# Kernel optimization log

Measured on AMD Instinct MI355X. Metric: run time of the kernel, lower is better.

## Reference

```python
import jax, jax.numpy as jnp
import numpy as np

H = 512          # hidden_size
FP = 256         # feature_padding
E = 512          # embedding_dim
NF = 768         # number of feature embeddings; num_features = NF + FP
L, B = 512, 32   # max_len, batch


def setup_inputs() -> dict:
    key = jax.random.key(0)
    ks = jax.random.split(key, 7)
    s = 0.02
    return {
        "feature_embeddings": jax.random.normal(ks[0], (NF, E), jnp.float32),
        "encoder_outputs": jax.random.normal(ks[1], (L, B, 2 * H), jnp.float32),
        "W_lin": jax.random.normal(ks[2], (H, 2 * H), jnp.float32) * s,   # linear_attn.weight
        "b_lin": jax.random.normal(ks[3], (H,), jnp.float32) * s,         # linear_attn.bias
        "W_feat": jax.random.normal(ks[4], (E, 2 * H), jnp.float32) * s,  # feature_attn.weight
        "b_feat": jax.random.normal(ks[5], (E,), jnp.float32) * s,        # feature_attn.bias
        "v": jax.random.normal(ks[6], (FP, H), jnp.float32) * s,          # self.v
    }


def reference(feature_embeddings, encoder_outputs, W_lin, b_lin, W_feat, b_feat, v):
    # encoder_outputs: [L, B, 2H]
    wh = jnp.einsum('lbi,hi->lbh', encoder_outputs, W_lin) + b_lin      # [L,B,H]
    vwh = jnp.einsum('fh,lbh->lbf', v, wh)                              # [L,B,FP]
    wh2 = jnp.einsum('lbi,ei->lbe', encoder_outputs, W_feat) + b_feat   # [L,B,E]
    fwh = jnp.einsum('ne,lbe->lbn', feature_embeddings, wh2)            # [L,B,NF]
    energy = jnp.concatenate([fwh, vwh], axis=-1)                       # [L,B,NF+FP]
    attn = jax.nn.softmax(energy, axis=-1)                              # softmax over features
    # attn_energies was [B, L, N]; .transpose(1,2) -> [B, N, L]
    return jnp.transpose(attn, (1, 2, 0))
```

## Files before the change

kernel.cpp:

```cpp
#include <hip/hip_runtime.h>
#include <hip/hip_bf16.h>
#include <math.h>

#define Hd   512
#define FPd  256
#define Ed   512
#define NFd  768
#define Ld   512
#define Bd   32
#define K2H  1024
#define Nd   1024
#define Md   (Ld * Bd)

typedef _Float16 f16x8  __attribute__((ext_vector_type(8)));
typedef _Float16 f16x4  __attribute__((ext_vector_type(4)));
typedef float    f32x4  __attribute__((ext_vector_type(4)));
typedef float    f32x16 __attribute__((ext_vector_type(16)));

__global__ __launch_bounds__(256)
void build_wpack(const float* __restrict__ F,
                 const float* __restrict__ Wf,
                 const float* __restrict__ V,
                 const float* __restrict__ Wl,
                 _Float16* __restrict__ Bh) {
    __shared__ float fs[32][64];
    __shared__ float wtile[32][36];
    const int tid = threadIdx.x;
    const int kx  = blockIdx.x;
    const int ny  = blockIdx.y;
    const int n0  = ny * 32;
    const int kl  = tid & 31;
    const int k   = kx * 32 + kl;
    const int ty  = tid >> 5;

    const float* src;  const float* wsrc;
    if (n0 < NFd) { src = F + (size_t)n0 * Ed;          wsrc = Wf; }
    else          { src = V + (size_t)(n0 - NFd) * Hd;  wsrc = Wl; }

    float acc[4];
#pragma unroll
    for (int i = 0; i < 4; i++) acc[i] = 0.f;

    for (int e0 = 0; e0 < 512; e0 += 64) {
#pragma unroll
        for (int rep = 0; rep < 2; rep++) {
            int idx = rep * 256 + tid;
            int i   = idx >> 4;
            int kq  = idx & 15;
            float4 v4 = *(const float4*)(src + (size_t)i * 512 + e0 + kq * 4);
            *(float4*)(&fs[i][kq * 4]) = v4;
        }
        __syncthreads();
#pragma unroll 4
        for (int kk = 0; kk < 64; kk += 4) {
            float w0 = wsrc[(size_t)(e0 + kk + 0) * K2H + k];
            float w1 = wsrc[(size_t)(e0 + kk + 1) * K2H + k];
            float w2 = wsrc[(size_t)(e0 + kk + 2) * K2H + k];
            float w3 = wsrc[(size_t)(e0 + kk + 3) * K2H + k];
#pragma unroll
            for (int i = 0; i < 4; i++) {
                float4 f4 = *(const float4*)(&fs[ty * 4 + i][kk]);
                acc[i] += f4.x * w0 + f4.y * w1 + f4.z * w2 + f4.w * w3;
            }
        }
        __syncthreads();
    }
#pragma unroll
    for (int i = 0; i < 4; i++) wtile[ty * 4 + i][kl] = acc[i];
    __syncthreads();
    if (tid < 128) {
        const int lane = tid & 63;
        const int ksl  = tid >> 6;
        const int nl   = lane & 31;
        const int kf   = ksl * 16 + (lane >> 5) * 8;
        float w[8];
        *(float4*)(w)     = *(const float4*)(&wtile[nl][kf]);
        *(float4*)(w + 4) = *(const float4*)(&wtile[nl][kf + 4]);
        f16x8 h;
#pragma unroll
        for (int j = 0; j < 8; j++) h[j] = (_Float16)w[j];
        const size_t fo = ((size_t)((ny * 64) + (kx * 2 + ksl)) * 64 + lane) * 8;
        *(f16x8*)(Bh + fo) = h;
    }
}

__global__ __launch_bounds__(64)
void build_bias(const float* __restrict__ F, const float* __restrict__ bf,
                const float* __restrict__ V, const float* __restrict__ bl,
                float* __restrict__ bias) {
    const int n    = blockIdx.x;
    const int lane = threadIdx.x;
    const float* row; const float* bsrc;
    if (n < NFd) { row = F + (size_t)n * Ed;          bsrc = bf; }
    else         { row = V + (size_t)(n - NFd) * Hd;  bsrc = bl; }
    float a = 0.f;
#pragma unroll
    for (int rep = 0; rep < 8; rep++) {
        int e = rep * 64 + lane;
        a += row[e] * bsrc[e];
    }
#pragma unroll
    for (int off = 1; off < 64; off <<= 1) a += __shfl_xor(a, off);
    if (lane == 0) bias[n] = a;
}

__global__ __launch_bounds__(1024)
void gemm_direct(const float* __restrict__ enc,
                 const _Float16* __restrict__ Bh,
                 const float* __restrict__ bias,
                 float* __restrict__ out) {
    __shared__ char AsB[2][8192];
    __shared__ float red[16][64];
    __shared__ float redc[64];

    const int tid  = threadIdx.x;
    const int lane = tid & 63;
    const int wn   = tid >> 6;
    const int hf   = lane >> 5;
    const int l31  = lane & 31;
    const int b    = blockIdx.x >> 3;
    const int l0   = (blockIdx.x & 7) * 64;

    float bv[2];
#pragma unroll
    for (int nt = 0; nt < 2; nt++) bv[nt] = bias[wn * 64 + nt * 32 + l31];
    f32x16 acc[2][2];
#pragma unroll
    for (int ms = 0; ms < 2; ms++)
#pragma unroll
        for (int nt = 0; nt < 2; nt++)
#pragma unroll
            for (int r = 0; r < 16; r++) acc[ms][nt][r] = bv[nt];

    const int srow = tid >> 4;
    const int skf  = (tid & 15) * 4;
    const float* gA = enc + ((size_t)(l0 + srow) * Bd + b) * K2H + skf;

    const int kk_w   = skf >> 4;
    const int lh_w   = (skf & 15) >> 3;
    const int j0_w   = skf & 7;
    const int lane_w = lh_w * 32 + (srow & 31);
    const int slot_w = lane_w ^ ((lane_w >> 3) & 7) ^ kk_w;
    const uint32_t wb = (uint32_t)((srow >> 5) * 4096 + kk_w * 1024 + slot_w * 16 + j0_w * 2);

    const uint32_t rb16 = (uint32_t)((lane ^ ((lane >> 3) & 7)) << 4);

    const _Float16* Bp0 = Bh + ((size_t)(wn * 2 + 0) * 64 * 64 + lane) * 8;
    const _Float16* Bp1 = Bh + ((size_t)(wn * 2 + 1) * 64 * 64 + lane) * 8;

#define STAGE_CHUNK(dst, p)                                               \
    {                                                                     \
        f16x4 h_;                                                         \
        _Pragma("unroll")                                                 \
        for (int j = 0; j < 4; j++) h_[j] = (_Float16)((p)[j]);           \
        *(f16x4*)((dst) + wb) = h_;                                       \
    }

    {
        f32x4 p0 = *(const f32x4*)gA;
        STAGE_CHUNK(AsB[0], p0)
    }
    f32x4 pf1 = *(const f32x4*)(gA + 64);
    f16x8 b_cur0 = *(const f16x8*)(Bp0);
    f16x8 b_cur1 = *(const f16x8*)(Bp1);

    for (int c = 0; c < 16; ++c) {
        __syncthreads();
        f32x4 pf2;
        if (c < 14) pf2 = *(const f32x4*)(gA + (c + 2) * 64);
        const char* hbase = AsB[c & 1];
#pragma unroll
        for (int kk = 0; kk < 4; ++kk) {
            const uint32_t ko = (uint32_t)(kk * 1024) + (rb16 ^ (uint32_t)(kk << 4));
            f16x8 a_h[2];
#pragma unroll
            for (int ms = 0; ms < 2; ms++)
                a_h[ms] = *(const f16x8*)(hbase + ms * 4096 + ko);
            int t = c * 4 + kk + 1;
            if (t > 63) t = 63;
            f16x8 b_nxt0 = *(const f16x8*)(Bp0 + (size_t)t * 512);
            f16x8 b_nxt1 = *(const f16x8*)(Bp1 + (size_t)t * 512);
            acc[0][0] = __builtin_amdgcn_mfma_f32_32x32x16_f16(a_h[0], b_cur0, acc[0][0], 0, 0, 0);
            acc[1][0] = __builtin_amdgcn_mfma_f32_32x32x16_f16(a_h[1], b_cur0, acc[1][0], 0, 0, 0);
            acc[0][1] = __builtin_amdgcn_mfma_f32_32x32x16_f16(a_h[0], b_cur1, acc[0][1], 0, 0, 0);
            acc[1][1] = __builtin_amdgcn_mfma_f32_32x32x16_f16(a_h[1], b_cur1, acc[1][1], 0, 0, 0);
            b_cur0 = b_nxt0;
            b_cur1 = b_nxt1;
        }
        if (c < 15) {
            STAGE_CHUNK(AsB[(c + 1) & 1], pf1)
            pf1 = pf2;
        }
    }

#pragma unroll
    for (int ms = 0; ms < 2; ms++) {
#pragma unroll
        for (int r = 0; r < 16; r++) {
            float mx = fmaxf(acc[ms][0][r], acc[ms][1][r]);
#pragma unroll
            for (int off = 1; off < 32; off <<= 1) mx = fmaxf(mx, __shfl_xor(mx, off));
            if (l31 == r) red[wn][ms * 32 + (r & 3) + 8 * (r >> 2) + 4 * hf] = mx;
        }
    }
    __syncthreads();
    if (tid < 64) {
        float v = red[0][tid];
#pragma unroll
        for (int w = 1; w < 16; w++) v = fmaxf(v, red[w][tid]);
        redc[tid] = v;
    }
    __syncthreads();

#pragma unroll
    for (int ms = 0; ms < 2; ms++) {
#pragma unroll
        for (int r = 0; r < 16; r++) {
            const int rr = ms * 32 + (r & 3) + 8 * (r >> 2) + 4 * hf;
            const float rm = redc[rr];
            float s = 0.f;
#pragma unroll
            for (int nt = 0; nt < 2; nt++) {
                float e = __expf(acc[ms][nt][r] - rm);
                acc[ms][nt][r] = e;
                s += e;
            }
#pragma unroll
            for (int off = 1; off < 32; off <<= 1) s += __shfl_xor(s, off);
            if (l31 == r) red[wn][rr] = s;
        }
    }
    __syncthreads();
    if (tid < 64) {
        float v = 0.f;
#pragma unroll
        for (int w = 0; w < 16; w++) v += red[w][tid];
        redc[tid] = 1.0f / v;
    }
    __syncthreads();

#pragma unroll
    for (int ms = 0; ms < 2; ms++) {
        float invr[16];
#pragma unroll
        for (int r = 0; r < 16; r++)
            invr[r] = redc[ms * 32 + (r & 3) + 8 * (r >> 2) + 4 * hf];
#pragma unroll
        for (int nt = 0; nt < 2; nt++) {
            const int n = wn * 64 + nt * 32 + l31;
            float* op = out + ((size_t)b * Nd + n) * Ld + l0 + ms * 32 + hf * 4;
#pragma unroll
            for (int g = 0; g < 4; g++) {
                float4 v = make_float4(acc[ms][nt][g * 4 + 0] * invr[g * 4 + 0],
                                       acc[ms][nt][g * 4 + 1] * invr[g * 4 + 1],
                                       acc[ms][nt][g * 4 + 2] * invr[g * 4 + 2],
                                       acc[ms][nt][g * 4 + 3] * invr[g * 4 + 3]);
                *(float4*)(op + 8 * g) = v;
            }
        }
    }
}

extern "C" void kernel_launch(void* const* d_in, const int* in_sizes, int n_in,
                              void* d_out, int out_size, void* d_ws, size_t ws_size,
                              hipStream_t stream) {
    (void)in_sizes; (void)n_in; (void)out_size; (void)ws_size;

    const float* F    = (const float*)d_in[0];
    const float* enc  = (const float*)d_in[1];
    const float* Wlin = (const float*)d_in[2];
    const float* blin = (const float*)d_in[3];
    const float* Wfea = (const float*)d_in[4];
    const float* bfea = (const float*)d_in[5];
    const float* V    = (const float*)d_in[6];
    float* out = (float*)d_out;

    char* ws = (char*)d_ws;
    float*    bias = (float*)ws;
    _Float16* Bh   = (_Float16*)(ws + 0x10000);

    build_wpack<<<dim3(32, 32), 256, 0, stream>>>(F, Wfea, V, Wlin, Bh);
    build_bias<<<dim3(1024), 64, 0, stream>>>(F, bfea, V, blin, bias);
    gemm_direct<<<dim3(256), 1024, 0, stream>>>(enc, Bh, bias, out);
}
```

Baseline: 111.2 us.

## Pre-convert encoder outputs to packed fp16 and merge prologue kernels

Adds a prologue stage that converts the fp32 encoder outputs into an fp16 layout already arranged in MFMA operand order. The GEMM then loads A fragments straight from global memory, which removes the shared-memory double buffering, the in-loop conversion and the barriers. The weight-pack and bias kernels are merged into the same launch, saving one kernel launch. In exchange there is an extra global round trip of a 32 MB fp16 copy of the activations, and the GEMM now depends on cache hits rather than LDS reuse.

Measured after the change: 132.1 us. 18.7% more time.

```diff
diff --git a/kernel.cpp b/kernel.cpp
--- a/kernel.cpp
+++ b/kernel.cpp
@@ -13,103 +13,145 @@
 #define Md   (Ld * Bd)
 
 typedef _Float16 f16x8  __attribute__((ext_vector_type(8)));
-typedef _Float16 f16x4  __attribute__((ext_vector_type(4)));
 typedef float    f32x4  __attribute__((ext_vector_type(4)));
 typedef float    f32x16 __attribute__((ext_vector_type(16)));
 
 __global__ __launch_bounds__(256)
-void build_wpack(const float* __restrict__ F,
-                 const float* __restrict__ Wf,
-                 const float* __restrict__ V,
-                 const float* __restrict__ Wl,
-                 _Float16* __restrict__ Bh) {
+void prologue(const float* __restrict__ enc,
+              const float* __restrict__ F,
+              const float* __restrict__ Wf,
+              const float* __restrict__ V,
+              const float* __restrict__ Wl,
+              const float* __restrict__ bf,
+              const float* __restrict__ bl,
+              _Float16* __restrict__ A16,
+              _Float16* __restrict__ Bh,
+              float* __restrict__ bias) {
     __shared__ float fs[32][64];
     __shared__ float wtile[32][36];
+    const int bid = blockIdx.x;
     const int tid = threadIdx.x;
-    const int kx  = blockIdx.x;
-    const int ny  = blockIdx.y;
-    const int n0  = ny * 32;
-    const int kl  = tid & 31;
-    const int k   = kx * 32 + kl;
-    const int ty  = tid >> 5;
-
-    const float* src;  const float* wsrc;
-    if (n0 < NFd) { src = F + (size_t)n0 * Ed;          wsrc = Wf; }
-    else          { src = V + (size_t)(n0 - NFd) * Hd;  wsrc = Wl; }
-
-    float acc[4];
-#pragma unroll
-    for (int i = 0; i < 4; i++) acc[i] = 0.f;
-
-    for (int e0 = 0; e0 < 512; e0 += 64) {
-#pragma unroll
-        for (int rep = 0; rep < 2; rep++) {
-            int idx = rep * 256 + tid;
-            int i   = idx >> 4;
-            int kq  = idx & 15;
-            float4 v4 = *(const float4*)(src + (size_t)i * 512 + e0 + kq * 4);
-            *(float4*)(&fs[i][kq * 4]) = v4;
-        }
+
+    if (bid < 1024) {
+        const int b    = bid >> 5;
+        const int rem  = bid & 31;
+        const int lc   = rem >> 2;
+        const int q    = rem & 3;
+        const int lane = tid & 63;
+        const int c    = q * 4 + (tid >> 6);
+        const int l31  = lane & 31;
+        const int hfk  = (lane >> 5) * 8;
+#pragma unroll
+        for (int ms = 0; ms < 2; ms++) {
+            const int l = lc * 64 + ms * 32 + l31;
+            const float* src = enc + ((size_t)l * Bd + b) * K2H;
+#pragma unroll
+            for (int kk = 0; kk < 4; kk++) {
+                const int k = c * 64 + kk * 16 + hfk;
+                f32x4 p0 = *(const f32x4*)(src + k);
+                f32x4 p1 = *(const f32x4*)(src + k + 4);
+                f16x8 h;
+                h[0] = (_Float16)p0[0]; h[1] = (_Float16)p0[1];
+                h[2] = (_Float16)p0[2]; h[3] = (_Float16)p0[3];
+                h[4] = (_Float16)p1[0]; h[5] = (_Float16)p1[1];
+                h[6] = (_Float16)p1[2]; h[7] = (_Float16)p1[3];
+                const size_t off =
+                    ((((size_t)(b * 8 + lc) * 16 + c) * 4 + kk) * 2 + ms) * 512
+                    + (size_t)lane * 8;
+                *(f16x8*)(A16 + off) = h;
+            }
+        }
+        return;
+    }
+
+    if (bid < 2048) {
+        const int r   = bid - 1024;
+        const int kx  = r & 31;
+        const int ny  = r >> 5;
+        const int n0  = ny * 32;
+        const int kl  = tid & 31;
+        const int k   = kx * 32 + kl;
+        const int ty  = tid >> 5;
+
+        const float* src;  const float* wsrc;
+        if (n0 < NFd) { src = F + (size_t)n0 * Ed;          wsrc = Wf; }
+        else          { src = V + (size_t)(n0 - NFd) * Hd;  wsrc = Wl; }
+
+        float acc[4];
+#pragma unroll
+        for (int i = 0; i < 4; i++) acc[i] = 0.f;
+
+        for (int e0 = 0; e0 < 512; e0 += 64) {
+#pragma unroll
+            for (int rep = 0; rep < 2; rep++) {
+                int idx = rep * 256 + tid;
+                int i   = idx >> 4;
+                int kq  = idx & 15;
+                float4 v4 = *(const float4*)(src + (size_t)i * 512 + e0 + kq * 4);
+                *(float4*)(&fs[i][kq * 4]) = v4;
+            }
+            __syncthreads();
+#pragma unroll 4
+            for (int kk = 0; kk < 64; kk += 4) {
+                float w0 = wsrc[(size_t)(e0 + kk + 0) * K2H + k];
+                float w1 = wsrc[(size_t)(e0 + kk + 1) * K2H + k];
+                float w2 = wsrc[(size_t)(e0 + kk + 2) * K2H + k];
+                float w3 = wsrc[(size_t)(e0 + kk + 3) * K2H + k];
+#pragma unroll
+                for (int i = 0; i < 4; i++) {
+                    float4 f4 = *(const float4*)(&fs[ty * 4 + i][kk]);
+                    acc[i] += f4.x * w0 + f4.y * w1 + f4.z * w2 + f4.w * w3;
+                }
+            }
+            __syncthreads();
+        }
+#pragma unroll
+        for (int i = 0; i < 4; i++) wtile[ty * 4 + i][kl] = acc[i];
         __syncthreads();
-#pragma unroll 4
-        for (int kk = 0; kk < 64; kk += 4) {
-            float w0 = wsrc[(size_t)(e0 + kk + 0) * K2H + k];
-            float w1 = wsrc[(size_t)(e0 + kk + 1) * K2H + k];
-            float w2 = wsrc[(size_t)(e0 + kk + 2) * K2H + k];
-            float w3 = wsrc[(size_t)(e0 + kk + 3) * K2H + k];
-#pragma unroll
-            for (int i = 0; i < 4; i++) {
-                float4 f4 = *(const float4*)(&fs[ty * 4 + i][kk]);
-                acc[i] += f4.x * w0 + f4.y * w1 + f4.z * w2 + f4.w * w3;
-            }
-        }
-        __syncthreads();
-    }
-#pragma unroll
-    for (int i = 0; i < 4; i++) wtile[ty * 4 + i][kl] = acc[i];
-    __syncthreads();
-    if (tid < 128) {
-        const int lane = tid & 63;
-        const int ksl  = tid >> 6;
-        const int nl   = lane & 31;
-        const int kf   = ksl * 16 + (lane >> 5) * 8;
-        float w[8];
-        *(float4*)(w)     = *(const float4*)(&wtile[nl][kf]);
-        *(float4*)(w + 4) = *(const float4*)(&wtile[nl][kf + 4]);
-        f16x8 h;
-#pragma unroll
-        for (int j = 0; j < 8; j++) h[j] = (_Float16)w[j];
-        const size_t fo = ((size_t)((ny * 64) + (kx * 2 + ksl)) * 64 + lane) * 8;
-        *(f16x8*)(Bh + fo) = h;
+        if (tid < 128) {
+            const int lane = tid & 63;
+            const int ksl  = tid >> 6;
+            const int nl   = lane & 31;
+            const int kf   = ksl * 16 + (lane >> 5) * 8;
+            float w[8];
+            *(float4*)(w)     = *(const float4*)(&wtile[nl][kf]);
+            *(float4*)(w + 4) = *(const float4*)(&wtile[nl][kf + 4]);
+            f16x8 h;
+#pragma unroll
+            for (int j = 0; j < 8; j++) h[j] = (_Float16)w[j];
+            const size_t fo = ((size_t)((ny * 64) + (kx * 2 + ksl)) * 64 + lane) * 8;
+            *(f16x8*)(Bh + fo) = h;
+        }
+        return;
+    }
+
+    {
+        const int n0 = (bid - 2048) * 64;
+        const int ng = tid >> 2;
+        const int p  = tid & 3;
+        const int n  = n0 + ng;
+        const float* row; const float* bsrc;
+        if (n < NFd) { row = F + (size_t)n * Ed;          bsrc = bf; }
+        else         { row = V + (size_t)(n - NFd) * Hd;  bsrc = bl; }
+        float a = 0.f;
+#pragma unroll
+        for (int i = 0; i < 32; i++) {
+            const int idx = i * 16 + p * 4;
+            f32x4 r4 = *(const f32x4*)(row + idx);
+            f32x4 s4 = *(const f32x4*)(bsrc + idx);
+            a += r4[0] * s4[0] + r4[1] * s4[1] + r4[2] * s4[2] + r4[3] * s4[3];
+        }
+        a += __shfl_xor(a, 1);
+        a += __shfl_xor(a, 2);
+        if (p == 0) bias[n] = a;
     }
 }
 
-__global__ __launch_bounds__(64)
-void build_bias(const float* __restrict__ F, const float* __restrict__ bf,
-                const float* __restrict__ V, const float* __restrict__ bl,
-                float* __restrict__ bias) {
-    const int n    = blockIdx.x;
-    const int lane = threadIdx.x;
-    const float* row; const float* bsrc;
-    if (n < NFd) { row = F + (size_t)n * Ed;          bsrc = bf; }
-    else         { row = V + (size_t)(n - NFd) * Hd;  bsrc = bl; }
-    float a = 0.f;
-#pragma unroll
-    for (int rep = 0; rep < 8; rep++) {
-        int e = rep * 64 + lane;
-        a += row[e] * bsrc[e];
-    }
-#pragma unroll
-    for (int off = 1; off < 64; off <<= 1) a += __shfl_xor(a, off);
-    if (lane == 0) bias[n] = a;
-}
-
 __global__ __launch_bounds__(1024)
-void gemm_direct(const float* __restrict__ enc,
+void gemm_direct(const _Float16* __restrict__ A16,
                  const _Float16* __restrict__ Bh,
                  const float* __restrict__ bias,
                  float* __restrict__ out) {
-    __shared__ char AsB[2][8192];
     __shared__ float red[16][64];
     __shared__ float redc[64];
 
@@ -132,65 +174,20 @@
 #pragma unroll
             for (int r = 0; r < 16; r++) acc[ms][nt][r] = bv[nt];
 
-    const int srow = tid >> 4;
-    const int skf  = (tid & 15) * 4;
-    const float* gA = enc + ((size_t)(l0 + srow) * Bd + b) * K2H + skf;
-
-    const int kk_w   = skf >> 4;
-    const int lh_w   = (skf & 15) >> 3;
-    const int j0_w   = skf & 7;
-    const int lane_w = lh_w * 32 + (srow & 31);
-    const int slot_w = lane_w ^ ((lane_w >> 3) & 7) ^ kk_w;
-    const uint32_t wb = (uint32_t)((srow >> 5) * 4096 + kk_w * 1024 + slot_w * 16 + j0_w * 2);
-
-    const uint32_t rb16 = (uint32_t)((lane ^ ((lane >> 3) & 7)) << 4);
-
-    const _Float16* Bp0 = Bh + ((size_t)(wn * 2 + 0) * 64 * 64 + lane) * 8;
-    const _Float16* Bp1 = Bh + ((size_t)(wn * 2 + 1) * 64 * 64 + lane) * 8;
-
-#define STAGE_CHUNK(dst, p)                                               \
-    {                                                                     \
-        f16x4 h_;                                                         \
-        _Pragma("unroll")                                                 \
-        for (int j = 0; j < 4; j++) h_[j] = (_Float16)((p)[j]);           \
-        *(f16x4*)((dst) + wb) = h_;                                       \
-    }
-
-    {
-        f32x4 p0 = *(const f32x4*)gA;
-        STAGE_CHUNK(AsB[0], p0)
-    }
-    f32x4 pf1 = *(const f32x4*)(gA + 64);
-    f16x8 b_cur0 = *(const f16x8*)(Bp0);
-    f16x8 b_cur1 = *(const f16x8*)(Bp1);
-
-    for (int c = 0; c < 16; ++c) {
-        __syncthreads();
-        f32x4 pf2;
-        if (c < 14) pf2 = *(const f32x4*)(gA + (c + 2) * 64);
-        const char* hbase = AsB[c & 1];
-#pragma unroll
-        for (int kk = 0; kk < 4; ++kk) {
-            const uint32_t ko = (uint32_t)(kk * 1024) + (rb16 ^ (uint32_t)(kk << 4));
-            f16x8 a_h[2];
-#pragma unroll
-            for (int ms = 0; ms < 2; ms++)
-                a_h[ms] = *(const f16x8*)(hbase + ms * 4096 + ko);
-            int t = c * 4 + kk + 1;
-            if (t > 63) t = 63;
-            f16x8 b_nxt0 = *(const f16x8*)(Bp0 + (size_t)t * 512);
-            f16x8 b_nxt1 = *(const f16x8*)(Bp1 + (size_t)t * 512);
-            acc[0][0] = __builtin_amdgcn_mfma_f32_32x32x16_f16(a_h[0], b_cur0, acc[0][0], 0, 0, 0);
-            acc[1][0] = __builtin_amdgcn_mfma_f32_32x32x16_f16(a_h[1], b_cur0, acc[1][0], 0, 0, 0);
-            acc[0][1] = __builtin_amdgcn_mfma_f32_32x32x16_f16(a_h[0], b_cur1, acc[0][1], 0, 0, 0);
-            acc[1][1] = __builtin_amdgcn_mfma_f32_32x32x16_f16(a_h[1], b_cur1, acc[1][1], 0, 0, 0);
-            b_cur0 = b_nxt0;
-            b_cur1 = b_nxt1;
-        }
-        if (c < 15) {
-            STAGE_CHUNK(AsB[(c + 1) & 1], pf1)
-            pf1 = pf2;
-        }
+    const _Float16* Apl = A16 + (size_t)blockIdx.x * 65536 + (size_t)lane * 8;
+    const _Float16* Bp0 = Bh + ((size_t)(wn * 2 + 0) * 4096 + lane) * 8;
+    const _Float16* Bp1 = Bh + ((size_t)(wn * 2 + 1) * 4096 + lane) * 8;
+
+#pragma unroll 2
+    for (int t = 0; t < 64; ++t) {
+        f16x8 a0 = *(const f16x8*)(Apl + (size_t)t * 1024);
+        f16x8 a1 = *(const f16x8*)(Apl + (size_t)t * 1024 + 512);
+        f16x8 b0 = *(const f16x8*)(Bp0 + (size_t)t * 512);
+        f16x8 b1 = *(const f16x8*)(Bp1 + (size_t)t * 512);
+        acc[0][0] = __builtin_amdgcn_mfma_f32_32x32x16_f16(a0, b0, acc[0][0], 0, 0, 0);
+        acc[1][0] = __builtin_amdgcn_mfma_f32_32x32x16_f16(a1, b0, acc[1][0], 0, 0, 0);
+        acc[0][1] = __builtin_amdgcn_mfma_f32_32x32x16_f16(a0, b1, acc[0][1], 0, 0, 0);
+        acc[1][1] = __builtin_amdgcn_mfma_f32_32x32x16_f16(a1, b1, acc[1][1], 0, 0, 0);
     }
 
 #pragma unroll
@@ -278,8 +275,9 @@
     char* ws = (char*)d_ws;
     float*    bias = (float*)ws;
     _Float16* Bh   = (_Float16*)(ws + 0x10000);
-
-    build_wpack<<<dim3(32, 32), 256, 0, stream>>>(F, Wfea, V, Wlin, Bh);
-    build_bias<<<dim3(1024), 64, 0, stream>>>(F, bfea, V, blin, bias);
-    gemm_direct<<<dim3(256), 1024, 0, stream>>>(enc, Bh, bias, out);
+    _Float16* A16  = (_Float16*)(ws + 0x210000);
+
+    prologue<<<dim3(2064), 256, 0, stream>>>(enc, F, Wfea, V, Wlin, bfea, blin,
+                                             A16, Bh, bias);
+    gemm_direct<<<dim3(256), 1024, 0, stream>>>(A16, Bh, bias, out);
 }
```

## Merge prologue kernels and deepen B prefetch in GEMM loop with setprio

Applied to the files above, without the earlier changes.

The weight-pack kernel and the bias kernel become one launch. The extra blocks compute bias dot products with vectorized loads, four threads per output. In the main GEMM loop, the B-fragment global prefetch now runs two steps ahead instead of one, the A prefetch distance drops from two chunks to one, and s_setprio is raised around the MFMA group. The aims are less launch overhead and better overlap of memory latency with matrix math. The unclamped prefetch index reads past the end of the packed B buffer on the last iterations. Those values are never used, but the reads go outside the intended buffer.

After: 118.2 us. 1.06x slower.

```diff
diff --git a/kernel.cpp b/kernel.cpp
--- a/kernel.cpp
+++ b/kernel.cpp
@@ -18,90 +18,99 @@
 typedef float    f32x16 __attribute__((ext_vector_type(16)));
 
 __global__ __launch_bounds__(256)
-void build_wpack(const float* __restrict__ F,
-                 const float* __restrict__ Wf,
-                 const float* __restrict__ V,
-                 const float* __restrict__ Wl,
-                 _Float16* __restrict__ Bh) {
+void prologue(const float* __restrict__ F,
+              const float* __restrict__ Wf,
+              const float* __restrict__ V,
+              const float* __restrict__ Wl,
+              const float* __restrict__ bf,
+              const float* __restrict__ bl,
+              _Float16* __restrict__ Bh,
+              float* __restrict__ bias) {
     __shared__ float fs[32][64];
     __shared__ float wtile[32][36];
+    const int bid = blockIdx.x;
     const int tid = threadIdx.x;
-    const int kx  = blockIdx.x;
-    const int ny  = blockIdx.y;
-    const int n0  = ny * 32;
-    const int kl  = tid & 31;
-    const int k   = kx * 32 + kl;
-    const int ty  = tid >> 5;
-
-    const float* src;  const float* wsrc;
-    if (n0 < NFd) { src = F + (size_t)n0 * Ed;          wsrc = Wf; }
-    else          { src = V + (size_t)(n0 - NFd) * Hd;  wsrc = Wl; }
-
-    float acc[4];
-#pragma unroll
-    for (int i = 0; i < 4; i++) acc[i] = 0.f;
-
-    for (int e0 = 0; e0 < 512; e0 += 64) {
-#pragma unroll
-        for (int rep = 0; rep < 2; rep++) {
-            int idx = rep * 256 + tid;
-            int i   = idx >> 4;
-            int kq  = idx & 15;
-            float4 v4 = *(const float4*)(src + (size_t)i * 512 + e0 + kq * 4);
-            *(float4*)(&fs[i][kq * 4]) = v4;
-        }
+
+    if (bid < 1024) {
+        const int kx  = bid & 31;
+        const int ny  = bid >> 5;
+        const int n0  = ny * 32;
+        const int kl  = tid & 31;
+        const int k   = kx * 32 + kl;
+        const int ty  = tid >> 5;
+
+        const float* src;  const float* wsrc;
+        if (n0 < NFd) { src = F + (size_t)n0 * Ed;          wsrc = Wf; }
+        else          { src = V + (size_t)(n0 - NFd) * Hd;  wsrc = Wl; }
+
+        float acc[4];
+#pragma unroll
+        for (int i = 0; i < 4; i++) acc[i] = 0.f;
+
+        for (int e0 = 0; e0 < 512; e0 += 64) {
+#pragma unroll
+            for (int rep = 0; rep < 2; rep++) {
+                int idx = rep * 256 + tid;
+                int i   = idx >> 4;
+                int kq  = idx & 15;
+                float4 v4 = *(const float4*)(src + (size_t)i * 512 + e0 + kq * 4);
+                *(float4*)(&fs[i][kq * 4]) = v4;
+            }
+            __syncthreads();
+#pragma unroll 4
+            for (int kk = 0; kk < 64; kk += 4) {
+                float w0 = wsrc[(size_t)(e0 + kk + 0) * K2H + k];
+                float w1 = wsrc[(size_t)(e0 + kk + 1) * K2H + k];
+                float w2 = wsrc[(size_t)(e0 + kk + 2) * K2H + k];
+                float w3 = wsrc[(size_t)(e0 + kk + 3) * K2H + k];
+#pragma unroll
+                for (int i = 0; i < 4; i++) {
+                    float4 f4 = *(const float4*)(&fs[ty * 4 + i][kk]);
+                    acc[i] += f4.x * w0 + f4.y * w1 + f4.z * w2 + f4.w * w3;
+                }
+            }
+            __syncthreads();
+        }
+#pragma unroll
+        for (int i = 0; i < 4; i++) wtile[ty * 4 + i][kl] = acc[i];
         __syncthreads();
-#pragma unroll 4
-        for (int kk = 0; kk < 64; kk += 4) {
-            float w0 = wsrc[(size_t)(e0 + kk + 0) * K2H + k];
-            float w1 = wsrc[(size_t)(e0 + kk + 1) * K2H + k];
-            float w2 = wsrc[(size_t)(e0 + kk + 2) * K2H + k];
-            float w3 = wsrc[(size_t)(e0 + kk + 3) * K2H + k];
-#pragma unroll
-            for (int i = 0; i < 4; i++) {
-                float4 f4 = *(const float4*)(&fs[ty * 4 + i][kk]);
-                acc[i] += f4.x * w0 + f4.y * w1 + f4.z * w2 + f4.w * w3;
-            }
-        }
-        __syncthreads();
-    }
-#pragma unroll
-    for (int i = 0; i < 4; i++) wtile[ty * 4 + i][kl] = acc[i];
-    __syncthreads();
-    if (tid < 128) {
-        const int lane = tid & 63;
-        const int ksl  = tid >> 6;
-        const int nl   = lane & 31;
-        const int kf   = ksl * 16 + (lane >> 5) * 8;
-        float w[8];
-        *(float4*)(w)     = *(const float4*)(&wtile[nl][kf]);
-        *(float4*)(w + 4) = *(const float4*)(&wtile[nl][kf + 4]);
-        f16x8 h;
-#pragma unroll
-        for (int j = 0; j < 8; j++) h[j] = (_Float16)w[j];
-        const size_t fo = ((size_t)((ny * 64) + (kx * 2 + ksl)) * 64 + lane) * 8;
-        *(f16x8*)(Bh + fo) = h;
-    }
-}
-
-__global__ __launch_bounds__(64)
-void build_bias(const float* __restrict__ F, const float* __restrict__ bf,
-                const float* __restrict__ V, const float* __restrict__ bl,
-                float* __restrict__ bias) {
-    const int n    = blockIdx.x;
-    const int lane = threadIdx.x;
-    const float* row; const float* bsrc;
-    if (n < NFd) { row = F + (size_t)n * Ed;          bsrc = bf; }
-    else         { row = V + (size_t)(n - NFd) * Hd;  bsrc = bl; }
-    float a = 0.f;
-#pragma unroll
-    for (int rep = 0; rep < 8; rep++) {
-        int e = rep * 64 + lane;
-        a += row[e] * bsrc[e];
-    }
-#pragma unroll
-    for (int off = 1; off < 64; off <<= 1) a += __shfl_xor(a, off);
-    if (lane == 0) bias[n] = a;
+        if (tid < 128) {
+            const int lane = tid & 63;
+            const int ksl  = tid >> 6;
+            const int nl   = lane & 31;
+            const int kf   = ksl * 16 + (lane >> 5) * 8;
+            float w[8];
+            *(float4*)(w)     = *(const float4*)(&wtile[nl][kf]);
+            *(float4*)(w + 4) = *(const float4*)(&wtile[nl][kf + 4]);
+            f16x8 h;
+#pragma unroll
+            for (int j = 0; j < 8; j++) h[j] = (_Float16)w[j];
+            const size_t fo = ((size_t)((ny * 64) + (kx * 2 + ksl)) * 64 + lane) * 8;
+            *(f16x8*)(Bh + fo) = h;
+        }
+        return;
+    }
+
+    {
+        const int n0 = (bid - 1024) * 64;
+        const int ng = tid >> 2;
+        const int p  = tid & 3;
+        const int n  = n0 + ng;
+        const float* row; const float* bsrc;
+        if (n < NFd) { row = F + (size_t)n * Ed;          bsrc = bf; }
+        else         { row = V + (size_t)(n - NFd) * Hd;  bsrc = bl; }
+        float a = 0.f;
+#pragma unroll
+        for (int i = 0; i < 32; i++) {
+            const int idx = i * 16 + p * 4;
+            f32x4 r4 = *(const f32x4*)(row + idx);
+            f32x4 s4 = *(const f32x4*)(bsrc + idx);
+            a += r4[0] * s4[0] + r4[1] * s4[1] + r4[2] * s4[2] + r4[3] * s4[3];
+        }
+        a += __shfl_xor(a, 1);
+        a += __shfl_xor(a, 2);
+        if (p == 0) bias[n] = a;
+    }
 }
 
 __global__ __launch_bounds__(1024)
@@ -145,8 +154,8 @@
 
     const uint32_t rb16 = (uint32_t)((lane ^ ((lane >> 3) & 7)) << 4);
 
-    const _Float16* Bp0 = Bh + ((size_t)(wn * 2 + 0) * 64 * 64 + lane) * 8;
-    const _Float16* Bp1 = Bh + ((size_t)(wn * 2 + 1) * 64 * 64 + lane) * 8;
+    const _Float16* Bp0 = Bh + ((size_t)(wn * 2 + 0) * 4096 + lane) * 8;
+    const _Float16* Bp1 = Bh + ((size_t)(wn * 2 + 1) * 4096 + lane) * 8;
 
 #define STAGE_CHUNK(dst, p)                                               \
     {                                                                     \
@@ -160,37 +169,34 @@
         f32x4 p0 = *(const f32x4*)gA;
         STAGE_CHUNK(AsB[0], p0)
     }
-    f32x4 pf1 = *(const f32x4*)(gA + 64);
     f16x8 b_cur0 = *(const f16x8*)(Bp0);
     f16x8 b_cur1 = *(const f16x8*)(Bp1);
+    f16x8 b_nx0  = *(const f16x8*)(Bp0 + 512);
+    f16x8 b_nx1  = *(const f16x8*)(Bp1 + 512);
 
     for (int c = 0; c < 16; ++c) {
         __syncthreads();
-        f32x4 pf2;
-        if (c < 14) pf2 = *(const f32x4*)(gA + (c + 2) * 64);
+        f32x4 pfA;
+        if (c < 15) pfA = *(const f32x4*)(gA + (c + 1) * 64);
         const char* hbase = AsB[c & 1];
 #pragma unroll
         for (int kk = 0; kk < 4; ++kk) {
             const uint32_t ko = (uint32_t)(kk * 1024) + (rb16 ^ (uint32_t)(kk << 4));
-            f16x8 a_h[2];
-#pragma unroll
-            for (int ms = 0; ms < 2; ms++)
-                a_h[ms] = *(const f16x8*)(hbase + ms * 4096 + ko);
-            int t = c * 4 + kk + 1;
-            if (t > 63) t = 63;
-            f16x8 b_nxt0 = *(const f16x8*)(Bp0 + (size_t)t * 512);
-            f16x8 b_nxt1 = *(const f16x8*)(Bp1 + (size_t)t * 512);
-            acc[0][0] = __builtin_amdgcn_mfma_f32_32x32x16_f16(a_h[0], b_cur0, acc[0][0], 0, 0, 0);
-            acc[1][0] = __builtin_amdgcn_mfma_f32_32x32x16_f16(a_h[1], b_cur0, acc[1][0], 0, 0, 0);
-            acc[0][1] = __builtin_amdgcn_mfma_f32_32x32x16_f16(a_h[0], b_cur1, acc[0][1], 0, 0, 0);
-            acc[1][1] = __builtin_amdgcn_mfma_f32_32x32x16_f16(a_h[1], b_cur1, acc[1][1], 0, 0, 0);
-            b_cur0 = b_nxt0;
-            b_cur1 = b_nxt1;
-        }
-        if (c < 15) {
-            STAGE_CHUNK(AsB[(c + 1) & 1], pf1)
-            pf1 = pf2;
-        }
+            f16x8 a0 = *(const f16x8*)(hbase + ko);
+            f16x8 a1 = *(const f16x8*)(hbase + 4096 + ko);
+            const size_t t2 = (size_t)(c * 4 + kk + 2) * 512;
+            f16x8 b_n20 = *(const f16x8*)(Bp0 + t2);
+            f16x8 b_n21 = *(const f16x8*)(Bp1 + t2);
+            __builtin_amdgcn_s_setprio(1);
+            acc[0][0] = __builtin_amdgcn_mfma_f32_32x32x16_f16(a0, b_cur0, acc[0][0], 0, 0, 0);
+            acc[1][0] = __builtin_amdgcn_mfma_f32_32x32x16_f16(a1, b_cur0, acc[1][0], 0, 0, 0);
+            acc[0][1] = __builtin_amdgcn_mfma_f32_32x32x16_f16(a0, b_cur1, acc[0][1], 0, 0, 0);
+            acc[1][1] = __builtin_amdgcn_mfma_f32_32x32x16_f16(a1, b_cur1, acc[1][1], 0, 0, 0);
+            __builtin_amdgcn_s_setprio(0);
+            b_cur0 = b_nx0; b_cur1 = b_nx1;
+            b_nx0 = b_n20;  b_nx1 = b_n21;
+        }
+        if (c < 15) STAGE_CHUNK(AsB[(c + 1) & 1], pfA)
     }
 
 #pragma unroll
@@ -279,7 +285,6 @@
     float*    bias = (float*)ws;
     _Float16* Bh   = (_Float16*)(ws + 0x10000);
 
-    build_wpack<<<dim3(32, 32), 256, 0, stream>>>(F, Wfea, V, Wlin, Bh);
-    build_bias<<<dim3(1024), 64, 0, stream>>>(F, bfea, V, blin, bias);
+    prologue<<<dim3(1040), 256, 0, stream>>>(F, Wfea, V, Wlin, bfea, blin, Bh, bias);
     gemm_direct<<<dim3(256), 1024, 0, stream>>>(enc, Bh, bias, out);
 }
```
